# Kernel optimization log

Measured on AMD Instinct MI355X. Metric: run time of the kernel, lower is better.

Reference implementation:

```python
import jax, jax.numpy as jnp
import numpy as np

BETA = 0.5

def setup_inputs() -> dict:
    key = jax.random.key(0)
    ks = jax.random.split(key, 12)
    B, H, d, hid = 2048, 100, 128, 256
    item_num, region_num, dist_num = 100000, 1000, 16
    return {
        "history": jax.random.randint(ks[0], (B, H), 0, item_num),
        "target": jax.random.randint(ks[1], (B,), 0, item_num),
        "history_region": jax.random.randint(ks[2], (B, H), 0, region_num),
        "target_region": jax.random.randint(ks[3], (B,), 0, region_num),
        "target_distance": jax.random.uniform(ks[4], (B,), dtype=jnp.float32),
        "E_hist": jax.random.normal(ks[5], (item_num, d), dtype=jnp.float32) * 0.01,
        "E_tgt": jax.random.normal(ks[6], (item_num, d), dtype=jnp.float32) * 0.01,
        "E_reg": jax.random.normal(ks[7], (region_num, d), dtype=jnp.float32) * 0.01,
        "E_dist": jax.random.normal(ks[8], (dist_num, d), dtype=jnp.float32) * 0.01,
        "W1": jax.random.normal(ks[9], (hid, 2 * d), dtype=jnp.float32) * 0.05,
        "b1": jnp.zeros((hid,), dtype=jnp.float32),
        "w2": jax.random.normal(ks[10], (hid,), dtype=jnp.float32) * 0.05,
    }

def reference(history, target, history_region, target_region, target_distance,
              E_hist, E_tgt, E_reg, E_dist, W1, b1, w2):
    # history embeddings: [B,H,2d]
    hist = jnp.concatenate([E_hist[history], E_reg[history_region]], axis=-1)
    # target embeddings: [B,1,2d]
    tgt = jnp.concatenate([E_tgt[target], E_reg[target_region]], axis=-1)[:, None, :]
    x = hist * tgt                                   # [B,H,2d]
    a = jax.nn.relu(jnp.einsum('bhd,kd->bhk', x, W1) + b1)  # [B,H,hid]
    score = jnp.einsum('bhk,k->bh', a, w2)           # [B,H]
    # distance bias: scalar per batch element
    dist = jnp.sum(target_distance[:, None] * E_dist[0], axis=1)  # [B]
    exp_A = jnp.exp(score + dist[:, None])           # [B,H]
    mask = (history != target[:, None]).astype(exp_A.dtype)
    exp_A = exp_A * mask
    exp_sum = jnp.power(jnp.sum(exp_A, axis=-1), BETA)  # [B]
    attn = exp_A / exp_sum[:, None]                  # [B,H]
    # weighted inner product: sum_h sum_d attn*hist*tgt
    pred = jnp.sum(hist * attn[:, :, None] * tgt, axis=(1, 2))  # [B]
    return jax.nn.sigmoid(pred)
```

## Files before the change

### kernel.cpp

```cpp
#include <hip/hip_runtime.h>
#include <stdint.h>

typedef __attribute__((ext_vector_type(8))) short bf16x8;
typedef __attribute__((ext_vector_type(4))) float f32x4;

#define HH  100
#define DD  128
#define HID 256

__device__ __forceinline__ unsigned short f2bf(float f) {
    unsigned int u = __float_as_uint(f);
    u += 0x7fffu + ((u >> 16) & 1u);
    return (unsigned short)(u >> 16);
}

__device__ __forceinline__ void load_lds_1k(const void* g, void* l) {
    __builtin_amdgcn_global_load_lds((const __attribute__((address_space(1))) unsigned int*)g,
                                     (__attribute__((address_space(3))) unsigned int*)l,
                                     16, 0, 0);
}

__global__ void w1_pack(const float* __restrict__ W1, unsigned short* __restrict__ W1p) {
    int unit = blockIdx.x * 256 + threadIdx.x;
    int lane = unit & 63;
    int s    = (unit >> 6) & 7;
    int st   = unit >> 9;
    int col  = lane & 15, quad = lane >> 4;
    const float* src = W1 + (size_t)(st * 16 + col) * HID + s * 32 + quad * 8;
    union { unsigned short u[8]; bf16x8 v; } o;
    #pragma unroll
    for (int j = 0; j < 8; j++) o.u[j] = f2bf(src[j]);
    *(bf16x8*)(W1p + (size_t)unit * 8) = o.v;
}

__global__ __launch_bounds__(256, 2) void nais_kernel(
    const int* __restrict__ history,
    const int* __restrict__ target,
    const int* __restrict__ history_region,
    const int* __restrict__ target_region,
    const float* __restrict__ target_distance,
    const float* __restrict__ E_hist,
    const float* __restrict__ E_tgt,
    const float* __restrict__ E_reg,
    const float* __restrict__ E_dist,
    const float* __restrict__ b1,
    const float* __restrict__ w2,
    const unsigned short* __restrict__ W1p,
    float* __restrict__ out)
{
    __shared__ __align__(16) unsigned short Bs[2][8192];
    __shared__ __align__(16) float tgts[HID];
    __shared__ __align__(16) float b1s[HID];
    __shared__ __align__(16) float w2s[HID];
    __shared__ float score[128];
    __shared__ float xsum[HH];
    __shared__ float eA[HH];
    __shared__ float exs[HH];
    __shared__ int hidx[HH];
    __shared__ int hreg[HH];
    __shared__ float s_sumE;

    const int b    = blockIdx.x;
    const int t    = threadIdx.x;
    const int lane = t & 63;
    const int wave = t >> 6;
    const int col  = lane & 15;
    const int quad = lane >> 4;

    const int   tg    = target[b];
    const float tdist = target_distance[b];

    if (t < HH) {
        hidx[t] = history[b * HH + t];
        hreg[t] = history_region[b * HH + t];
    }
    if (wave == 1) {
        float v = E_dist[lane] + E_dist[64 + lane];
        #pragma unroll
        for (int off = 32; off; off >>= 1) v += __shfl_xor(v, off);
        if (lane == 0) s_sumE = v;
    }
    if (wave == 2) {
        float4 v;
        if (lane < 32) v = *(const float4*)(E_tgt + (size_t)tg * DD + lane * 4);
        else           v = *(const float4*)(E_reg + (size_t)target_region[b] * DD + (lane - 32) * 4);
        *(float4*)(tgts + lane * 4) = v;
    }
    if (wave == 3) {
        *(float4*)(b1s + lane * 4) = *(const float4*)(b1 + lane * 4);
        *(float4*)(w2s + lane * 4) = *(const float4*)(w2 + lane * 4);
    }
    __syncthreads();

    {
        const char* g = (const char*)W1p + wave * 4096 + lane * 16;
        char*       l = (char*)&Bs[0][0] + wave * 4096;
        #pragma unroll
        for (int i = 0; i < 4; i++) load_lds_1k(g + i * 1024, l + i * 1024);
    }

    bf16x8 afrag[2][8];
    float xs[2];
    #pragma unroll
    for (int mt = 0; mt < 2; mt++) {
        const int  row   = wave * 32 + mt * 16 + col;
        const bool valid = row < HH;
        const int  rc    = valid ? row : 0;
        const int  ih    = hidx[rc];
        const int  ir    = hreg[rc];
        const float* ph  = E_hist + (size_t)ih * DD + quad * 8;
        const float* pr  = E_reg  + (size_t)ir * DD + quad * 8;
        float acc = 0.f;
        #pragma unroll
        for (int c = 0; c < 2; c++) {
            #pragma unroll
            for (int si = 0; si < 4; si++) {
                const int s = c * 4 + si;
                const float* src = (s < 4) ? (ph + s * 32) : (pr + (s - 4) * 32);
                float4 v0 = {0.f, 0.f, 0.f, 0.f}, v1 = {0.f, 0.f, 0.f, 0.f};
                if (valid) { v0 = *(const float4*)src; v1 = *(const float4*)(src + 4); }
                const float* tp = tgts + s * 32 + quad * 8;
                float4 t0 = *(const float4*)tp, t1 = *(const float4*)(tp + 4);
                float x0 = v0.x * t0.x, x1 = v0.y * t0.y, x2 = v0.z * t0.z, x3 = v0.w * t0.w;
                float x4 = v1.x * t1.x, x5 = v1.y * t1.y, x6 = v1.z * t1.z, x7 = v1.w * t1.w;
                acc += (x0 + x1) + (x2 + x3) + ((x4 + x5) + (x6 + x7));
                union { unsigned short u[8]; bf16x8 v; } fb;
                fb.u[0] = f2bf(x0); fb.u[1] = f2bf(x1); fb.u[2] = f2bf(x2); fb.u[3] = f2bf(x3);
                fb.u[4] = f2bf(x4); fb.u[5] = f2bf(x5); fb.u[6] = f2bf(x6); fb.u[7] = f2bf(x7);
                afrag[mt][s] = fb.v;
            }
            asm volatile("" ::: "memory");
        }
        xs[mt] = acc;
    }
    #pragma unroll
    for (int mt = 0; mt < 2; mt++) {
        float v = xs[mt];
        v += __shfl_xor(v, 16);
        v += __shfl_xor(v, 32);
        const int row = wave * 32 + mt * 16 + col;
        if (quad == 0 && row < HH) xsum[row] = v;
    }

    float sacc[2][4] = {};
    #pragma unroll 1
    for (int k = 0; k < 8; k++) {
        __syncthreads();
        if (k < 7) {
            const char* g = (const char*)W1p + (k + 1) * 16384 + wave * 4096 + lane * 16;
            char*       l = (char*)&Bs[(k + 1) & 1][0] + wave * 4096;
            #pragma unroll
            for (int i = 0; i < 4; i++) load_lds_1k(g + i * 1024, l + i * 1024);
        }
        const unsigned short* buf = &Bs[k & 1][0];
        #pragma unroll
        for (int sti = 0; sti < 2; sti++) {
            const int st = k * 2 + sti;
            const float bb = b1s[st * 16 + col];
            const float ww = w2s[st * 16 + col];
            f32x4 acc0 = {0.f, 0.f, 0.f, 0.f};
            f32x4 acc1 = {0.f, 0.f, 0.f, 0.f};
            #pragma unroll
            for (int s = 0; s < 8; s++) {
                bf16x8 bfrag = *(const bf16x8*)(buf + ((sti * 8 + s) * 64 + lane) * 8);
                acc0 = __builtin_amdgcn_mfma_f32_16x16x32_bf16(afrag[0][s], bfrag, acc0, 0, 0, 0);
                acc1 = __builtin_amdgcn_mfma_f32_16x16x32_bf16(afrag[1][s], bfrag, acc1, 0, 0, 0);
            }
            #pragma unroll
            for (int r = 0; r < 4; r++) {
                float z0 = acc0[r] + bb; sacc[0][r] += (z0 > 0.f) ? z0 * ww : 0.f;
                float z1 = acc1[r] + bb; sacc[1][r] += (z1 > 0.f) ? z1 * ww : 0.f;
            }
        }
    }
    #pragma unroll
    for (int mt = 0; mt < 2; mt++) {
        #pragma unroll
        for (int r = 0; r < 4; r++) {
            float z = sacc[mt][r];
            z += __shfl_xor(z, 1);
            z += __shfl_xor(z, 2);
            z += __shfl_xor(z, 4);
            z += __shfl_xor(z, 8);
            sacc[mt][r] = z;
        }
    }
    if (col == 0) {
        #pragma unroll
        for (int mt = 0; mt < 2; mt++)
            #pragma unroll
            for (int r = 0; r < 4; r++)
                score[wave * 32 + mt * 16 + quad * 4 + r] = sacc[mt][r];
    }

    __syncthreads();

    const float dist = tdist * s_sumE;
    if (t < HH) {
        float e = (hidx[t] != tg) ? expf(score[t] + dist) : 0.f;
        eA[t]  = e;
        exs[t] = e * xsum[t];
    }
    __syncthreads();
    if (t < 64) {
        float s1 = eA[t]  + ((t + 64 < HH) ? eA[t + 64]  : 0.f);
        float s2 = exs[t] + ((t + 64 < HH) ? exs[t + 64] : 0.f);
        #pragma unroll
        for (int off = 32; off; off >>= 1) {
            s1 += __shfl_xor(s1, off);
            s2 += __shfl_xor(s2, off);
        }
        if (t == 0) {
            float pred = s2 / sqrtf(s1);
            out[b] = 1.f / (1.f + expf(-pred));
        }
    }
}

extern "C" void kernel_launch(void* const* d_in, const int* in_sizes, int n_in,
                              void* d_out, int out_size, void* d_ws, size_t ws_size,
                              hipStream_t stream) {
    const int*   history         = (const int*)d_in[0];
    const int*   target          = (const int*)d_in[1];
    const int*   history_region  = (const int*)d_in[2];
    const int*   target_region   = (const int*)d_in[3];
    const float* target_distance = (const float*)d_in[4];
    const float* E_hist          = (const float*)d_in[5];
    const float* E_tgt           = (const float*)d_in[6];
    const float* E_reg           = (const float*)d_in[7];
    const float* E_dist          = (const float*)d_in[8];
    const float* W1              = (const float*)d_in[9];
    const float* b1              = (const float*)d_in[10];
    const float* w2              = (const float*)d_in[11];

    unsigned short* W1p = (unsigned short*)d_ws;
    const int B = in_sizes[1];

    w1_pack<<<32, 256, 0, stream>>>(W1, W1p);
    nais_kernel<<<B, 256, 0, stream>>>(history, target, history_region, target_region,
                                       target_distance, E_hist, E_tgt, E_reg, E_dist,
                                       b1, w2, W1p, (float*)d_out);
}
```

Measured before the change: 203.1 us.

## Process two batch elements per block to share W1 tiles in LDS

Each 512-thread block now handles two batch elements, with each wave covering 16 history rows for both. A single W1 fragment read from LDS feeds MFMAs for both elements, and the W1 stream through LDS is amortized over two elements. This halves W1 global traffic and LDS fill work per element, but raises per-block resource use and tightens the register budget under the new launch bounds.

```diff
diff --git a/kernel.cpp b/kernel.cpp
--- a/kernel.cpp
+++ b/kernel.cpp
@@ -33,7 +33,7 @@
     *(bf16x8*)(W1p + (size_t)unit * 8) = o.v;
 }
 
-__global__ __launch_bounds__(256, 2) void nais_kernel(
+__global__ __launch_bounds__(512, 2) void nais_kernel(
     const int* __restrict__ history,
     const int* __restrict__ target,
     const int* __restrict__ history_region,
@@ -49,16 +49,18 @@
     float* __restrict__ out)
 {
     __shared__ __align__(16) unsigned short Bs[2][8192];
-    __shared__ __align__(16) float tgts[HID];
+    __shared__ __align__(16) float tgts[2][HID];
     __shared__ __align__(16) float b1s[HID];
     __shared__ __align__(16) float w2s[HID];
-    __shared__ float score[128];
-    __shared__ float xsum[HH];
-    __shared__ float eA[HH];
-    __shared__ float exs[HH];
-    __shared__ int hidx[HH];
-    __shared__ int hreg[HH];
+    __shared__ float score[2][128];
+    __shared__ float xsum[2][HH];
+    __shared__ float eA[2][HH];
+    __shared__ float exs[2][HH];
+    __shared__ int hidx[2][HH];
+    __shared__ int hreg[2][HH];
     __shared__ float s_sumE;
+    __shared__ float tds[2];
+    __shared__ int   tgs[2];
 
     const int b    = blockIdx.x;
     const int t    = threadIdx.x;
@@ -66,50 +68,55 @@
     const int wave = t >> 6;
     const int col  = lane & 15;
     const int quad = lane >> 4;
-
-    const int   tg    = target[b];
-    const float tdist = target_distance[b];
-
-    if (t < HH) {
-        hidx[t] = history[b * HH + t];
-        hreg[t] = history_region[b * HH + t];
-    }
-    if (wave == 1) {
-        float v = E_dist[lane] + E_dist[64 + lane];
-        #pragma unroll
-        for (int off = 32; off; off >>= 1) v += __shfl_xor(v, off);
-        if (lane == 0) s_sumE = v;
-    }
-    if (wave == 2) {
+    const int el   = t >> 8;
+    const int tt   = t & 255;
+
+    if (tt < HH) {
+        hidx[el][tt] = history[(2 * b + el) * HH + tt];
+        hreg[el][tt] = history_region[(2 * b + el) * HH + tt];
+    }
+    if (t < 2) {
+        tds[t] = target_distance[2 * b + t];
+        tgs[t] = target[2 * b + t];
+    }
+    if ((wave & 3) == 2) {
+        const int e  = wave >> 2;
+        const int tg = target[2 * b + e];
         float4 v;
         if (lane < 32) v = *(const float4*)(E_tgt + (size_t)tg * DD + lane * 4);
-        else           v = *(const float4*)(E_reg + (size_t)target_region[b] * DD + (lane - 32) * 4);
-        *(float4*)(tgts + lane * 4) = v;
+        else           v = *(const float4*)(E_reg + (size_t)target_region[2 * b + e] * DD + (lane - 32) * 4);
+        *(float4*)(tgts[e] + lane * 4) = v;
     }
     if (wave == 3) {
         *(float4*)(b1s + lane * 4) = *(const float4*)(b1 + lane * 4);
         *(float4*)(w2s + lane * 4) = *(const float4*)(w2 + lane * 4);
     }
+    if (wave == 7) {
+        float v = E_dist[lane] + E_dist[64 + lane];
+        #pragma unroll
+        for (int off = 32; off; off >>= 1) v += __shfl_xor(v, off);
+        if (lane == 0) s_sumE = v;
+    }
     __syncthreads();
 
     {
-        const char* g = (const char*)W1p + wave * 4096 + lane * 16;
-        char*       l = (char*)&Bs[0][0] + wave * 4096;
-        #pragma unroll
-        for (int i = 0; i < 4; i++) load_lds_1k(g + i * 1024, l + i * 1024);
+        const char* g = (const char*)W1p + wave * 2048 + lane * 16;
+        char*       l = (char*)&Bs[0][0] + wave * 2048;
+        load_lds_1k(g, l);
+        load_lds_1k(g + 1024, l + 1024);
     }
 
     bf16x8 afrag[2][8];
     float xs[2];
-    #pragma unroll
-    for (int mt = 0; mt < 2; mt++) {
-        const int  row   = wave * 32 + mt * 16 + col;
-        const bool valid = row < HH;
-        const int  rc    = valid ? row : 0;
-        const int  ih    = hidx[rc];
-        const int  ir    = hreg[rc];
-        const float* ph  = E_hist + (size_t)ih * DD + quad * 8;
-        const float* pr  = E_reg  + (size_t)ir * DD + quad * 8;
+    const int  row   = wave * 16 + col;
+    const bool valid = row < HH;
+    const int  rc    = valid ? row : 0;
+    #pragma unroll
+    for (int e = 0; e < 2; e++) {
+        const int  ih   = hidx[e][rc];
+        const int  ir   = hreg[e][rc];
+        const float* ph = E_hist + (size_t)ih * DD + quad * 8;
+        const float* pr = E_reg  + (size_t)ir * DD + quad * 8;
         float acc = 0.f;
         #pragma unroll
         for (int c = 0; c < 2; c++) {
@@ -119,7 +126,7 @@
                 const float* src = (s < 4) ? (ph + s * 32) : (pr + (s - 4) * 32);
                 float4 v0 = {0.f, 0.f, 0.f, 0.f}, v1 = {0.f, 0.f, 0.f, 0.f};
                 if (valid) { v0 = *(const float4*)src; v1 = *(const float4*)(src + 4); }
-                const float* tp = tgts + s * 32 + quad * 8;
+                const float* tp = tgts[e] + s * 32 + quad * 8;
                 float4 t0 = *(const float4*)tp, t1 = *(const float4*)(tp + 4);
                 float x0 = v0.x * t0.x, x1 = v0.y * t0.y, x2 = v0.z * t0.z, x3 = v0.w * t0.w;
                 float x4 = v1.x * t1.x, x5 = v1.y * t1.y, x6 = v1.z * t1.z, x7 = v1.w * t1.w;
@@ -127,19 +134,18 @@
                 union { unsigned short u[8]; bf16x8 v; } fb;
                 fb.u[0] = f2bf(x0); fb.u[1] = f2bf(x1); fb.u[2] = f2bf(x2); fb.u[3] = f2bf(x3);
                 fb.u[4] = f2bf(x4); fb.u[5] = f2bf(x5); fb.u[6] = f2bf(x6); fb.u[7] = f2bf(x7);
-                afrag[mt][s] = fb.v;
+                afrag[e][s] = fb.v;
             }
             asm volatile("" ::: "memory");
         }
-        xs[mt] = acc;
-    }
-    #pragma unroll
-    for (int mt = 0; mt < 2; mt++) {
-        float v = xs[mt];
+        xs[e] = acc;
+    }
+    #pragma unroll
+    for (int e = 0; e < 2; e++) {
+        float v = xs[e];
         v += __shfl_xor(v, 16);
         v += __shfl_xor(v, 32);
-        const int row = wave * 32 + mt * 16 + col;
-        if (quad == 0 && row < HH) xsum[row] = v;
+        if (quad == 0 && valid) xsum[e][row] = v;
     }
 
     float sacc[2][4] = {};
@@ -147,10 +153,10 @@
     for (int k = 0; k < 8; k++) {
         __syncthreads();
         if (k < 7) {
-            const char* g = (const char*)W1p + (k + 1) * 16384 + wave * 4096 + lane * 16;
-            char*       l = (char*)&Bs[(k + 1) & 1][0] + wave * 4096;
-            #pragma unroll
-            for (int i = 0; i < 4; i++) load_lds_1k(g + i * 1024, l + i * 1024);
+            const char* g = (const char*)W1p + (k + 1) * 16384 + wave * 2048 + lane * 16;
+            char*       l = (char*)&Bs[(k + 1) & 1][0] + wave * 2048;
+            load_lds_1k(g, l);
+            load_lds_1k(g + 1024, l + 1024);
         }
         const unsigned short* buf = &Bs[k & 1][0];
         #pragma unroll
@@ -174,45 +180,45 @@
         }
     }
     #pragma unroll
-    for (int mt = 0; mt < 2; mt++) {
+    for (int e = 0; e < 2; e++) {
         #pragma unroll
         for (int r = 0; r < 4; r++) {
-            float z = sacc[mt][r];
+            float z = sacc[e][r];
             z += __shfl_xor(z, 1);
             z += __shfl_xor(z, 2);
             z += __shfl_xor(z, 4);
             z += __shfl_xor(z, 8);
-            sacc[mt][r] = z;
+            sacc[e][r] = z;
         }
     }
     if (col == 0) {
         #pragma unroll
-        for (int mt = 0; mt < 2; mt++)
+        for (int e = 0; e < 2; e++)
             #pragma unroll
             for (int r = 0; r < 4; r++)
-                score[wave * 32 + mt * 16 + quad * 4 + r] = sacc[mt][r];
+                score[e][wave * 16 + quad * 4 + r] = sacc[e][r];
     }
 
     __syncthreads();
 
-    const float dist = tdist * s_sumE;
-    if (t < HH) {
-        float e = (hidx[t] != tg) ? expf(score[t] + dist) : 0.f;
-        eA[t]  = e;
-        exs[t] = e * xsum[t];
+    if (tt < HH) {
+        const float dist = tds[el] * s_sumE;
+        float e = (hidx[el][tt] != tgs[el]) ? expf(score[el][tt] + dist) : 0.f;
+        eA[el][tt]  = e;
+        exs[el][tt] = e * xsum[el][tt];
     }
     __syncthreads();
-    if (t < 64) {
-        float s1 = eA[t]  + ((t + 64 < HH) ? eA[t + 64]  : 0.f);
-        float s2 = exs[t] + ((t + 64 < HH) ? exs[t + 64] : 0.f);
+    if (tt < 64) {
+        float s1 = eA[el][tt]  + ((tt + 64 < HH) ? eA[el][tt + 64]  : 0.f);
+        float s2 = exs[el][tt] + ((tt + 64 < HH) ? exs[el][tt + 64] : 0.f);
         #pragma unroll
         for (int off = 32; off; off >>= 1) {
             s1 += __shfl_xor(s1, off);
             s2 += __shfl_xor(s2, off);
         }
-        if (t == 0) {
+        if (tt == 0) {
             float pred = s2 / sqrtf(s1);
-            out[b] = 1.f / (1.f + expf(-pred));
+            out[2 * b + el] = 1.f / (1.f + expf(-pred));
         }
     }
 }
@@ -237,7 +243,7 @@
     const int B = in_sizes[1];
 
     w1_pack<<<32, 256, 0, stream>>>(W1, W1p);
-    nais_kernel<<<B, 256, 0, stream>>>(history, target, history_region, target_region,
-                                       target_distance, E_hist, E_tgt, E_reg, E_dist,
-                                       b1, w2, W1p, (float*)d_out);
-}
+    nais_kernel<<<B / 2, 512, 0, stream>>>(history, target, history_region, target_region,
+                                           target_distance, E_hist, E_tgt, E_reg, E_dist,
+                                           b1, w2, W1p, (float*)d_out);
+}
```

Measured after the change: 218.3 us. 1.07x slower.

## Keep full packed W1 in LDS and process eight batch rows per block

Applied to the files above, without the earlier changes.

Each 1024-thread block now stages the whole bf16-packed W1 (128 KB) into LDS once. Its 16 waves then handle eight batch elements in two rounds of four, one group of waves per element. This replaces per-element blocks that each streamed W1 through a double-buffered LDS pipeline, cutting repeated W1 traffic from L2 and per-k-step barriers. The cost is one large block per CU with no overlap of the initial W1 load, and possible register pressure under the 1024-thread launch bound. The softmax tail is reduced to one wave per element and reads history directly from global memory.

```diff
diff --git a/kernel.cpp b/kernel.cpp
--- a/kernel.cpp
+++ b/kernel.cpp
@@ -33,7 +33,7 @@
     *(bf16x8*)(W1p + (size_t)unit * 8) = o.v;
 }
 
-__global__ __launch_bounds__(256, 2) void nais_kernel(
+__global__ __launch_bounds__(1024) void nais_kernel(
     const int* __restrict__ history,
     const int* __restrict__ target,
     const int* __restrict__ history_region,
@@ -46,173 +46,181 @@
     const float* __restrict__ b1,
     const float* __restrict__ w2,
     const unsigned short* __restrict__ W1p,
-    float* __restrict__ out)
+    float* __restrict__ out,
+    int Btot)
 {
-    __shared__ __align__(16) unsigned short Bs[2][8192];
-    __shared__ __align__(16) float tgts[HID];
+    __shared__ __align__(16) unsigned short Bf[65536];
+    __shared__ __align__(16) float tgts[2][4][HID];
     __shared__ __align__(16) float b1s[HID];
     __shared__ __align__(16) float w2s[HID];
-    __shared__ float score[128];
-    __shared__ float xsum[HH];
-    __shared__ float eA[HH];
-    __shared__ float exs[HH];
-    __shared__ int hidx[HH];
-    __shared__ int hreg[HH];
+    __shared__ float score4[2][4][128];
+    __shared__ float xsum4[2][4][128];
     __shared__ float s_sumE;
 
-    const int b    = blockIdx.x;
+    const int blk  = blockIdx.x;
     const int t    = threadIdx.x;
     const int lane = t & 63;
     const int wave = t >> 6;
+    const int p    = wave & 3;
+    const int g    = wave >> 2;
     const int col  = lane & 15;
     const int quad = lane >> 4;
 
-    const int   tg    = target[b];
-    const float tdist = target_distance[b];
-
-    if (t < HH) {
-        hidx[t] = history[b * HH + t];
-        hreg[t] = history_region[b * HH + t];
-    }
-    if (wave == 1) {
+    {
+        const char* gp = (const char*)W1p + wave * 8192 + lane * 16;
+        char*       lp = (char*)&Bf[0] + wave * 8192 + lane * 16 - lane * 16;
+        lp = (char*)&Bf[0] + wave * 8192;
+        #pragma unroll
+        for (int i = 0; i < 8; i++) load_lds_1k(gp + i * 1024, lp + i * 1024);
+    }
+    if (p == 1) {
+        int e0 = blk * 8 + g; if (e0 >= Btot) e0 = Btot - 1;
+        const int tg0 = target[e0], tr0 = target_region[e0];
+        float4 v;
+        if (lane < 32) v = *(const float4*)(E_tgt + (size_t)tg0 * DD + lane * 4);
+        else           v = *(const float4*)(E_reg + (size_t)tr0 * DD + (lane - 32) * 4);
+        *(float4*)(&tgts[0][g][lane * 4]) = v;
+    }
+    if (wave == 2) {
+        *(float4*)(b1s + lane * 4) = *(const float4*)(b1 + lane * 4);
+        *(float4*)(w2s + lane * 4) = *(const float4*)(w2 + lane * 4);
+    }
+    if (wave == 3) {
         float v = E_dist[lane] + E_dist[64 + lane];
         #pragma unroll
         for (int off = 32; off; off >>= 1) v += __shfl_xor(v, off);
         if (lane == 0) s_sumE = v;
     }
-    if (wave == 2) {
-        float4 v;
-        if (lane < 32) v = *(const float4*)(E_tgt + (size_t)tg * DD + lane * 4);
-        else           v = *(const float4*)(E_reg + (size_t)target_region[b] * DD + (lane - 32) * 4);
-        *(float4*)(tgts + lane * 4) = v;
-    }
-    if (wave == 3) {
-        *(float4*)(b1s + lane * 4) = *(const float4*)(b1 + lane * 4);
-        *(float4*)(w2s + lane * 4) = *(const float4*)(w2 + lane * 4);
-    }
     __syncthreads();
 
-    {
-        const char* g = (const char*)W1p + wave * 4096 + lane * 16;
-        char*       l = (char*)&Bs[0][0] + wave * 4096;
-        #pragma unroll
-        for (int i = 0; i < 4; i++) load_lds_1k(g + i * 1024, l + i * 1024);
-    }
-
-    bf16x8 afrag[2][8];
-    float xs[2];
-    #pragma unroll
-    for (int mt = 0; mt < 2; mt++) {
-        const int  row   = wave * 32 + mt * 16 + col;
-        const bool valid = row < HH;
-        const int  rc    = valid ? row : 0;
-        const int  ih    = hidx[rc];
-        const int  ir    = hreg[rc];
-        const float* ph  = E_hist + (size_t)ih * DD + quad * 8;
-        const float* pr  = E_reg  + (size_t)ir * DD + quad * 8;
-        float acc = 0.f;
-        #pragma unroll
-        for (int c = 0; c < 2; c++) {
-            #pragma unroll
-            for (int si = 0; si < 4; si++) {
-                const int s = c * 4 + si;
-                const float* src = (s < 4) ? (ph + s * 32) : (pr + (s - 4) * 32);
-                float4 v0 = {0.f, 0.f, 0.f, 0.f}, v1 = {0.f, 0.f, 0.f, 0.f};
-                if (valid) { v0 = *(const float4*)src; v1 = *(const float4*)(src + 4); }
-                const float* tp = tgts + s * 32 + quad * 8;
-                float4 t0 = *(const float4*)tp, t1 = *(const float4*)(tp + 4);
-                float x0 = v0.x * t0.x, x1 = v0.y * t0.y, x2 = v0.z * t0.z, x3 = v0.w * t0.w;
-                float x4 = v1.x * t1.x, x5 = v1.y * t1.y, x6 = v1.z * t1.z, x7 = v1.w * t1.w;
-                acc += (x0 + x1) + (x2 + x3) + ((x4 + x5) + (x6 + x7));
-                union { unsigned short u[8]; bf16x8 v; } fb;
-                fb.u[0] = f2bf(x0); fb.u[1] = f2bf(x1); fb.u[2] = f2bf(x2); fb.u[3] = f2bf(x3);
-                fb.u[4] = f2bf(x4); fb.u[5] = f2bf(x5); fb.u[6] = f2bf(x6); fb.u[7] = f2bf(x7);
-                afrag[mt][s] = fb.v;
-            }
-            asm volatile("" ::: "memory");
-        }
-        xs[mt] = acc;
-    }
-    #pragma unroll
-    for (int mt = 0; mt < 2; mt++) {
-        float v = xs[mt];
-        v += __shfl_xor(v, 16);
-        v += __shfl_xor(v, 32);
-        const int row = wave * 32 + mt * 16 + col;
-        if (quad == 0 && row < HH) xsum[row] = v;
-    }
-
-    float sacc[2][4] = {};
     #pragma unroll 1
-    for (int k = 0; k < 8; k++) {
-        __syncthreads();
-        if (k < 7) {
-            const char* g = (const char*)W1p + (k + 1) * 16384 + wave * 4096 + lane * 16;
-            char*       l = (char*)&Bs[(k + 1) & 1][0] + wave * 4096;
-            #pragma unroll
-            for (int i = 0; i < 4; i++) load_lds_1k(g + i * 1024, l + i * 1024);
-        }
-        const unsigned short* buf = &Bs[k & 1][0];
-        #pragma unroll
-        for (int sti = 0; sti < 2; sti++) {
-            const int st = k * 2 + sti;
+    for (int r = 0; r < 2; r++) {
+        const int par = r & 1;
+        int e = blk * 8 + r * 4 + g; if (e >= Btot) e = Btot - 1;
+
+        const int row0 = p * 32 + col,       rc0 = (row0 < HH) ? row0 : row0 - 64;
+        const int row1 = p * 32 + 16 + col,  rc1 = (row1 < HH) ? row1 : row1 - 64;
+        const int ih0 = history[(size_t)e * HH + rc0];
+        const int ir0 = history_region[(size_t)e * HH + rc0];
+        const int ih1 = history[(size_t)e * HH + rc1];
+        const int ir1 = history_region[(size_t)e * HH + rc1];
+
+        bf16x8 afrag[2][8];
+        float xs[2];
+        #pragma unroll
+        for (int mt = 0; mt < 2; mt++) {
+            const float* ph = E_hist + (size_t)(mt ? ih1 : ih0) * DD + quad * 8;
+            const float* pr = E_reg  + (size_t)(mt ? ir1 : ir0) * DD + quad * 8;
+            float acc = 0.f;
+            #pragma unroll
+            for (int c = 0; c < 2; c++) {
+                #pragma unroll
+                for (int si = 0; si < 4; si++) {
+                    const int s = c * 4 + si;
+                    const float* src = (s < 4) ? (ph + s * 32) : (pr + (s - 4) * 32);
+                    float4 v0 = *(const float4*)src;
+                    float4 v1 = *(const float4*)(src + 4);
+                    const float* tp = &tgts[par][g][s * 32 + quad * 8];
+                    float4 t0 = *(const float4*)tp, t1 = *(const float4*)(tp + 4);
+                    float x0 = v0.x * t0.x, x1 = v0.y * t0.y, x2 = v0.z * t0.z, x3 = v0.w * t0.w;
+                    float x4 = v1.x * t1.x, x5 = v1.y * t1.y, x6 = v1.z * t1.z, x7 = v1.w * t1.w;
+                    acc += (x0 + x1) + (x2 + x3) + ((x4 + x5) + (x6 + x7));
+                    union { unsigned short u[8]; bf16x8 v; } fb;
+                    fb.u[0] = f2bf(x0); fb.u[1] = f2bf(x1); fb.u[2] = f2bf(x2); fb.u[3] = f2bf(x3);
+                    fb.u[4] = f2bf(x4); fb.u[5] = f2bf(x5); fb.u[6] = f2bf(x6); fb.u[7] = f2bf(x7);
+                    afrag[mt][s] = fb.v;
+                }
+                asm volatile("" ::: "memory");
+            }
+            xs[mt] = acc;
+        }
+        #pragma unroll
+        for (int mt = 0; mt < 2; mt++) {
+            float v = xs[mt];
+            v += __shfl_xor(v, 16);
+            v += __shfl_xor(v, 32);
+            if (quad == 0) xsum4[par][g][p * 32 + mt * 16 + col] = v;
+        }
+
+        float sacc[2][4] = {};
+        #pragma unroll 4
+        for (int st = 0; st < 16; st++) {
             const float bb = b1s[st * 16 + col];
             const float ww = w2s[st * 16 + col];
             f32x4 acc0 = {0.f, 0.f, 0.f, 0.f};
             f32x4 acc1 = {0.f, 0.f, 0.f, 0.f};
             #pragma unroll
             for (int s = 0; s < 8; s++) {
-                bf16x8 bfrag = *(const bf16x8*)(buf + ((sti * 8 + s) * 64 + lane) * 8);
+                bf16x8 bfrag = *(const bf16x8*)(Bf + ((st * 8 + s) * 64 + lane) * 8);
                 acc0 = __builtin_amdgcn_mfma_f32_16x16x32_bf16(afrag[0][s], bfrag, acc0, 0, 0, 0);
                 acc1 = __builtin_amdgcn_mfma_f32_16x16x32_bf16(afrag[1][s], bfrag, acc1, 0, 0, 0);
             }
             #pragma unroll
-            for (int r = 0; r < 4; r++) {
-                float z0 = acc0[r] + bb; sacc[0][r] += (z0 > 0.f) ? z0 * ww : 0.f;
-                float z1 = acc1[r] + bb; sacc[1][r] += (z1 > 0.f) ? z1 * ww : 0.f;
-            }
-        }
-    }
-    #pragma unroll
-    for (int mt = 0; mt < 2; mt++) {
-        #pragma unroll
-        for (int r = 0; r < 4; r++) {
-            float z = sacc[mt][r];
-            z += __shfl_xor(z, 1);
-            z += __shfl_xor(z, 2);
-            z += __shfl_xor(z, 4);
-            z += __shfl_xor(z, 8);
-            sacc[mt][r] = z;
-        }
-    }
-    if (col == 0) {
-        #pragma unroll
-        for (int mt = 0; mt < 2; mt++)
-            #pragma unroll
-            for (int r = 0; r < 4; r++)
-                score[wave * 32 + mt * 16 + quad * 4 + r] = sacc[mt][r];
-    }
-
-    __syncthreads();
-
-    const float dist = tdist * s_sumE;
-    if (t < HH) {
-        float e = (hidx[t] != tg) ? expf(score[t] + dist) : 0.f;
-        eA[t]  = e;
-        exs[t] = e * xsum[t];
-    }
-    __syncthreads();
-    if (t < 64) {
-        float s1 = eA[t]  + ((t + 64 < HH) ? eA[t + 64]  : 0.f);
-        float s2 = exs[t] + ((t + 64 < HH) ? exs[t + 64] : 0.f);
-        #pragma unroll
-        for (int off = 32; off; off >>= 1) {
-            s1 += __shfl_xor(s1, off);
-            s2 += __shfl_xor(s2, off);
-        }
-        if (t == 0) {
-            float pred = s2 / sqrtf(s1);
-            out[b] = 1.f / (1.f + expf(-pred));
+            for (int rr = 0; rr < 4; rr++) {
+                float z0 = acc0[rr] + bb; sacc[0][rr] += (z0 > 0.f) ? z0 * ww : 0.f;
+                float z1 = acc1[rr] + bb; sacc[1][rr] += (z1 > 0.f) ? z1 * ww : 0.f;
+            }
+        }
+        #pragma unroll
+        for (int mt = 0; mt < 2; mt++) {
+            #pragma unroll
+            for (int rr = 0; rr < 4; rr++) {
+                float z = sacc[mt][rr];
+                z += __shfl_xor(z, 1);
+                z += __shfl_xor(z, 2);
+                z += __shfl_xor(z, 4);
+                z += __shfl_xor(z, 8);
+                sacc[mt][rr] = z;
+            }
+        }
+        if (col == 0) {
+            #pragma unroll
+            for (int mt = 0; mt < 2; mt++)
+                #pragma unroll
+                for (int rr = 0; rr < 4; rr++)
+                    score4[par][g][p * 32 + mt * 16 + quad * 4 + rr] = sacc[mt][rr];
+        }
+
+        if (r == 0 && p == 1) {
+            int e1 = blk * 8 + 4 + g; if (e1 >= Btot) e1 = Btot - 1;
+            const int tg1 = target[e1], tr1 = target_region[e1];
+            float4 v;
+            if (lane < 32) v = *(const float4*)(E_tgt + (size_t)tg1 * DD + lane * 4);
+            else           v = *(const float4*)(E_reg + (size_t)tr1 * DD + (lane - 32) * 4);
+            *(float4*)(&tgts[1][g][lane * 4]) = v;
+        }
+
+        __syncthreads();
+
+        if (p == 0) {
+            const int eo = blk * 8 + r * 4 + g;
+            if (eo < Btot) {
+                const int   tg = target[eo];
+                const float td = target_distance[eo];
+                const float dist = td * s_sumE;
+                float sc1 = score4[par][g][lane];
+                float xv1 = xsum4[par][g][lane];
+                int   hi1 = history[(size_t)eo * HH + lane];
+                float e1 = (hi1 != tg) ? expf(sc1 + dist) : 0.f;
+                float e2 = 0.f, xv2 = 0.f;
+                if (lane + 64 < HH) {
+                    float sc2 = score4[par][g][lane + 64];
+                    xv2 = xsum4[par][g][lane + 64];
+                    int hi2 = history[(size_t)eo * HH + lane + 64];
+                    e2 = (hi2 != tg) ? expf(sc2 + dist) : 0.f;
+                }
+                float s1 = e1 + e2;
+                float s2 = e1 * xv1 + e2 * xv2;
+                #pragma unroll
+                for (int off = 32; off; off >>= 1) {
+                    s1 += __shfl_xor(s1, off);
+                    s2 += __shfl_xor(s2, off);
+                }
+                if (lane == 0) {
+                    float pred = s2 / sqrtf(s1);
+                    out[eo] = 1.f / (1.f + expf(-pred));
+                }
+            }
         }
     }
 }
@@ -235,9 +243,10 @@
 
     unsigned short* W1p = (unsigned short*)d_ws;
     const int B = in_sizes[1];
+    const int blocks = (B + 7) / 8;
 
     w1_pack<<<32, 256, 0, stream>>>(W1, W1p);
-    nais_kernel<<<B, 256, 0, stream>>>(history, target, history_region, target_region,
-                                       target_distance, E_hist, E_tgt, E_reg, E_dist,
-                                       b1, w2, W1p, (float*)d_out);
-}
+    nais_kernel<<<blocks, 1024, 0, stream>>>(history, target, history_region, target_region,
+                                             target_distance, E_hist, E_tgt, E_reg, E_dist,
+                                             b1, w2, W1p, (float*)d_out, B);
+}
```

Result: slower. 276.4 us (+36.1%).

## Split block across 8 waves with one 16-row M-tile per wave

Applied to the files above, without the earlier changes.

Doubles the block to 512 threads so each wave handles a single 16-row tile of history items instead of two. The per-wave register footprint for A fragments and accumulators halves, and each wave loads half of the W1 slice into LDS. Rows past 100 are padded by recomputing valid rows instead of zero-filling. The goal is more waves in flight to hide the latency of the gathered embedding loads, at the cost of more waves per block contending at each barrier.

```diff
diff --git a/kernel.cpp b/kernel.cpp
--- a/kernel.cpp
+++ b/kernel.cpp
@@ -33,7 +33,7 @@
     *(bf16x8*)(W1p + (size_t)unit * 8) = o.v;
 }
 
-__global__ __launch_bounds__(256, 2) void nais_kernel(
+__global__ __launch_bounds__(512, 4) void nais_kernel(
     const int* __restrict__ history,
     const int* __restrict__ target,
     const int* __restrict__ history_region,
@@ -53,7 +53,7 @@
     __shared__ __align__(16) float b1s[HID];
     __shared__ __align__(16) float w2s[HID];
     __shared__ float score[128];
-    __shared__ float xsum[HH];
+    __shared__ float xsum[128];
     __shared__ float eA[HH];
     __shared__ float exs[HH];
     __shared__ int hidx[HH];
@@ -74,83 +74,75 @@
         hidx[t] = history[b * HH + t];
         hreg[t] = history_region[b * HH + t];
     }
-    if (wave == 1) {
-        float v = E_dist[lane] + E_dist[64 + lane];
-        #pragma unroll
-        for (int off = 32; off; off >>= 1) v += __shfl_xor(v, off);
-        if (lane == 0) s_sumE = v;
-    }
-    if (wave == 2) {
+    if (wave == 4) {
         float4 v;
         if (lane < 32) v = *(const float4*)(E_tgt + (size_t)tg * DD + lane * 4);
         else           v = *(const float4*)(E_reg + (size_t)target_region[b] * DD + (lane - 32) * 4);
         *(float4*)(tgts + lane * 4) = v;
     }
-    if (wave == 3) {
+    if (wave == 5) {
         *(float4*)(b1s + lane * 4) = *(const float4*)(b1 + lane * 4);
         *(float4*)(w2s + lane * 4) = *(const float4*)(w2 + lane * 4);
     }
+    if (wave == 6) {
+        float v = E_dist[lane] + E_dist[64 + lane];
+        #pragma unroll
+        for (int off = 32; off; off >>= 1) v += __shfl_xor(v, off);
+        if (lane == 0) s_sumE = v;
+    }
     __syncthreads();
 
     {
-        const char* g = (const char*)W1p + wave * 4096 + lane * 16;
-        char*       l = (char*)&Bs[0][0] + wave * 4096;
-        #pragma unroll
-        for (int i = 0; i < 4; i++) load_lds_1k(g + i * 1024, l + i * 1024);
-    }
-
-    bf16x8 afrag[2][8];
-    float xs[2];
+        const char* g = (const char*)W1p + wave * 2048 + lane * 16;
+        char*       l = (char*)&Bs[0][0] + wave * 2048;
+        load_lds_1k(g, l);
+        load_lds_1k(g + 1024, l + 1024);
+    }
+
+    const int row = wave * 16 + col;
+    const int rc  = (row < HH) ? row : row - 64;
+    const int ih  = hidx[rc];
+    const int ir  = hreg[rc];
+    const float* ph = E_hist + (size_t)ih * DD + quad * 8;
+    const float* pr = E_reg  + (size_t)ir * DD + quad * 8;
+    bf16x8 afrag[8];
+    float acc = 0.f;
     #pragma unroll
-    for (int mt = 0; mt < 2; mt++) {
-        const int  row   = wave * 32 + mt * 16 + col;
-        const bool valid = row < HH;
-        const int  rc    = valid ? row : 0;
-        const int  ih    = hidx[rc];
-        const int  ir    = hreg[rc];
-        const float* ph  = E_hist + (size_t)ih * DD + quad * 8;
-        const float* pr  = E_reg  + (size_t)ir * DD + quad * 8;
-        float acc = 0.f;
-        #pragma unroll
-        for (int c = 0; c < 2; c++) {
-            #pragma unroll
-            for (int si = 0; si < 4; si++) {
-                const int s = c * 4 + si;
-                const float* src = (s < 4) ? (ph + s * 32) : (pr + (s - 4) * 32);
-                float4 v0 = {0.f, 0.f, 0.f, 0.f}, v1 = {0.f, 0.f, 0.f, 0.f};
-                if (valid) { v0 = *(const float4*)src; v1 = *(const float4*)(src + 4); }
-                const float* tp = tgts + s * 32 + quad * 8;
-                float4 t0 = *(const float4*)tp, t1 = *(const float4*)(tp + 4);
-                float x0 = v0.x * t0.x, x1 = v0.y * t0.y, x2 = v0.z * t0.z, x3 = v0.w * t0.w;
-                float x4 = v1.x * t1.x, x5 = v1.y * t1.y, x6 = v1.z * t1.z, x7 = v1.w * t1.w;
-                acc += (x0 + x1) + (x2 + x3) + ((x4 + x5) + (x6 + x7));
-                union { unsigned short u[8]; bf16x8 v; } fb;
-                fb.u[0] = f2bf(x0); fb.u[1] = f2bf(x1); fb.u[2] = f2bf(x2); fb.u[3] = f2bf(x3);
-                fb.u[4] = f2bf(x4); fb.u[5] = f2bf(x5); fb.u[6] = f2bf(x6); fb.u[7] = f2bf(x7);
-                afrag[mt][s] = fb.v;
-            }
-            asm volatile("" ::: "memory");
-        }
-        xs[mt] = acc;
-    }
-    #pragma unroll
-    for (int mt = 0; mt < 2; mt++) {
-        float v = xs[mt];
+    for (int c = 0; c < 2; c++) {
+        #pragma unroll
+        for (int si = 0; si < 4; si++) {
+            const int s = c * 4 + si;
+            const float* src = (s < 4) ? (ph + s * 32) : (pr + (s - 4) * 32);
+            float4 v0 = *(const float4*)src;
+            float4 v1 = *(const float4*)(src + 4);
+            const float* tp = tgts + s * 32 + quad * 8;
+            float4 t0 = *(const float4*)tp, t1 = *(const float4*)(tp + 4);
+            float x0 = v0.x * t0.x, x1 = v0.y * t0.y, x2 = v0.z * t0.z, x3 = v0.w * t0.w;
+            float x4 = v1.x * t1.x, x5 = v1.y * t1.y, x6 = v1.z * t1.z, x7 = v1.w * t1.w;
+            acc += (x0 + x1) + (x2 + x3) + ((x4 + x5) + (x6 + x7));
+            union { unsigned short u[8]; bf16x8 v; } fb;
+            fb.u[0] = f2bf(x0); fb.u[1] = f2bf(x1); fb.u[2] = f2bf(x2); fb.u[3] = f2bf(x3);
+            fb.u[4] = f2bf(x4); fb.u[5] = f2bf(x5); fb.u[6] = f2bf(x6); fb.u[7] = f2bf(x7);
+            afrag[s] = fb.v;
+        }
+        asm volatile("" ::: "memory");
+    }
+    {
+        float v = acc;
         v += __shfl_xor(v, 16);
         v += __shfl_xor(v, 32);
-        const int row = wave * 32 + mt * 16 + col;
-        if (quad == 0 && row < HH) xsum[row] = v;
-    }
-
-    float sacc[2][4] = {};
+        if (quad == 0) xsum[row] = v;
+    }
+
+    float sacc[4] = {};
     #pragma unroll 1
     for (int k = 0; k < 8; k++) {
         __syncthreads();
         if (k < 7) {
-            const char* g = (const char*)W1p + (k + 1) * 16384 + wave * 4096 + lane * 16;
-            char*       l = (char*)&Bs[(k + 1) & 1][0] + wave * 4096;
-            #pragma unroll
-            for (int i = 0; i < 4; i++) load_lds_1k(g + i * 1024, l + i * 1024);
+            const char* g = (const char*)W1p + (k + 1) * 16384 + wave * 2048 + lane * 16;
+            char*       l = (char*)&Bs[(k + 1) & 1][0] + wave * 2048;
+            load_lds_1k(g, l);
+            load_lds_1k(g + 1024, l + 1024);
         }
         const unsigned short* buf = &Bs[k & 1][0];
         #pragma unroll
@@ -159,38 +151,31 @@
             const float bb = b1s[st * 16 + col];
             const float ww = w2s[st * 16 + col];
             f32x4 acc0 = {0.f, 0.f, 0.f, 0.f};
-            f32x4 acc1 = {0.f, 0.f, 0.f, 0.f};
             #pragma unroll
             for (int s = 0; s < 8; s++) {
                 bf16x8 bfrag = *(const bf16x8*)(buf + ((sti * 8 + s) * 64 + lane) * 8);
-                acc0 = __builtin_amdgcn_mfma_f32_16x16x32_bf16(afrag[0][s], bfrag, acc0, 0, 0, 0);
-                acc1 = __builtin_amdgcn_mfma_f32_16x16x32_bf16(afrag[1][s], bfrag, acc1, 0, 0, 0);
+                acc0 = __builtin_amdgcn_mfma_f32_16x16x32_bf16(afrag[s], bfrag, acc0, 0, 0, 0);
             }
             #pragma unroll
             for (int r = 0; r < 4; r++) {
-                float z0 = acc0[r] + bb; sacc[0][r] += (z0 > 0.f) ? z0 * ww : 0.f;
-                float z1 = acc1[r] + bb; sacc[1][r] += (z1 > 0.f) ? z1 * ww : 0.f;
+                float z = acc0[r] + bb;
+                sacc[r] += (z > 0.f) ? z * ww : 0.f;
             }
         }
     }
     #pragma unroll
-    for (int mt = 0; mt < 2; mt++) {
-        #pragma unroll
-        for (int r = 0; r < 4; r++) {
-            float z = sacc[mt][r];
-            z += __shfl_xor(z, 1);
-            z += __shfl_xor(z, 2);
-            z += __shfl_xor(z, 4);
-            z += __shfl_xor(z, 8);
-            sacc[mt][r] = z;
-        }
+    for (int r = 0; r < 4; r++) {
+        float z = sacc[r];
+        z += __shfl_xor(z, 1);
+        z += __shfl_xor(z, 2);
+        z += __shfl_xor(z, 4);
+        z += __shfl_xor(z, 8);
+        sacc[r] = z;
     }
     if (col == 0) {
         #pragma unroll
-        for (int mt = 0; mt < 2; mt++)
-            #pragma unroll
-            for (int r = 0; r < 4; r++)
-                score[wave * 32 + mt * 16 + quad * 4 + r] = sacc[mt][r];
+        for (int r = 0; r < 4; r++)
+            score[wave * 16 + quad * 4 + r] = sacc[r];
     }
 
     __syncthreads();
@@ -237,7 +222,7 @@
     const int B = in_sizes[1];
 
     w1_pack<<<32, 256, 0, stream>>>(W1, W1p);
-    nais_kernel<<<B, 256, 0, stream>>>(history, target, history_region, target_region,
+    nais_kernel<<<B, 512, 0, stream>>>(history, target, history_region, target_region,
                                        target_distance, E_hist, E_tgt, E_reg, E_dist,
                                        b1, w2, W1p, (float*)d_out);
 }
```

Result: faster. 192.6 us (-5.1%).
